# Kernel optimization log

Measured on AMD Instinct MI355X. Metric: run time of the kernel, lower is better.

## Reference

```python
import jax, jax.numpy as jnp
import numpy as np

N_USERS = 50000
N_ENTITIES = 100000
N_EDGES = 2000000
NNZ = 1000000
N_REL = 17  # n_relations; weight has n_relations-1 = 16 rows
DIM = 64
N_HOPS = 3


def setup_inputs() -> dict:
    key = jax.random.key(0)
    ks = jax.random.split(key, 8)
    user_emb = jax.random.normal(ks[0], (N_USERS, DIM), dtype=jnp.float32)
    entity_emb = jax.random.normal(ks[1], (N_ENTITIES, DIM), dtype=jnp.float32)
    weight = jax.random.normal(ks[2], (N_REL - 1, DIM), dtype=jnp.float32)
    unmask = jax.random.uniform(ks[3], (N_EDGES,), dtype=jnp.float32)
    edge_index = jax.random.randint(ks[4], (2, N_EDGES), 0, N_ENTITIES, dtype=jnp.int64) if jax.config.jax_enable_x64 else jax.random.randint(ks[4], (2, N_EDGES), 0, N_ENTITIES).astype(jnp.int32)
    edge_type = jax.random.randint(ks[5], (N_EDGES,), 1, N_REL).astype(edge_index.dtype)
    interact_rows = jax.random.randint(ks[6], (NNZ,), 0, N_USERS).astype(edge_index.dtype)
    interact_cols = jax.random.randint(ks[7], (NNZ,), 0, N_ENTITIES).astype(edge_index.dtype)
    return {
        "user_emb": user_emb,
        "entity_emb": entity_emb,
        "weight": weight,
        "unmask": unmask,
        "edge_index": edge_index,
        "edge_type": edge_type,
        "interact_rows": interact_rows,
        "interact_cols": interact_cols,
    }


def _l2_normalize(x, eps=1e-12):
    # matches torch.nn.functional.normalize(dim=1)
    norm = jnp.sqrt(jnp.sum(x * x, axis=1, keepdims=True))
    return x / jnp.maximum(norm, eps)


def reference(user_emb, entity_emb, weight, unmask, edge_index, edge_type, interact_rows, interact_cols):
    """GraphConv.forward with mess_dropout=False, node_dropout=False (eval math)."""
    head = edge_index[0]
    tail = edge_index[1]
    rel_emb = weight[edge_type - 1]                      # [E, D] gather
    entity_res = entity_emb
    user_res = user_emb
    ent = entity_emb
    for _ in range(N_HOPS):
        # KG aggregate: gather-multiply-scatter_sum
        neigh = ent[tail] * unmask[:, None] * rel_emb    # [E, D]
        ent_agg = jax.ops.segment_sum(neigh, head, num_segments=N_ENTITIES)
        # user aggregate: sparse (unit-valued COO) mm -> gather + segment_sum
        usr_agg = jax.ops.segment_sum(ent[interact_cols], interact_rows, num_segments=N_USERS)
        ent = _l2_normalize(ent_agg)
        usr = _l2_normalize(usr_agg)
        entity_res = entity_res + ent
        user_res = user_res + usr
    return entity_res, user_res
```

## Files before the change

### kernel.cpp

```cpp
#include <hip/hip_runtime.h>
#include <hip/hip_fp16.h>
#include <math.h>

#define N_USERS   50000
#define N_ENT     100000
#define N_EDGES   2000000
#define NNZ       1000000
#define DIM       64
#define N_HOPS    3
#define HALF_E    (N_ENT / 2)
#define HALF_U    (N_USERS / 2)

#define GA     512
#define NB_E   ((N_ENT + 255) >> 8)
#define NB_U   ((N_USERS + 255) >> 8)
#define CAP_D  6400


__device__ inline unsigned pack_h2(float x, float y) {
    unsigned lo = __half_as_ushort(__float2half_rn(x));
    unsigned hi = __half_as_ushort(__float2half_rn(y));
    return lo | (hi << 16);
}

__device__ inline float2 unpack_h2(unsigned u) {
    __half2 h = *reinterpret_cast<__half2*>(&u);
    return __half22float2(h);
}

__global__ void f32_to_f16(const float4* __restrict__ in, uint4* __restrict__ out, int n4) {
    int i = blockIdx.x * blockDim.x + threadIdx.x;
    if (i < n4) {
        float4 a = in[2 * i], b = in[2 * i + 1];
        uint4 o;
        o.x = pack_h2(a.x, a.y);
        o.y = pack_h2(a.z, a.w);
        o.z = pack_h2(b.x, b.y);
        o.w = pack_h2(b.z, b.w);
        out[i] = o;
    }
}


template <int NBUCKET>
__global__ __launch_bounds__(256) void bucket_hist(const int* __restrict__ key, int n,
                                                   int* __restrict__ bh) {
    __shared__ int h[NBUCKET];
    for (int t = threadIdx.x; t < NBUCKET; t += 256) h[t] = 0;
    __syncthreads();
    int chunk = (n + GA - 1) / GA;
    int s = blockIdx.x * chunk;
    int e = n < s + chunk ? n : s + chunk;
    for (int i = s + threadIdx.x; i < e; i += 256)
        atomicAdd(&h[key[i] >> 8], 1);
    __syncthreads();
    for (int t = threadIdx.x; t < NBUCKET; t += 256)
        bh[t * GA + blockIdx.x] = h[t];
}

__global__ void scan_partial(const int* __restrict__ cnt, int n, int* __restrict__ bsum) {
    __shared__ int sd[256];
    int tid = threadIdx.x, i = blockIdx.x * 256 + tid;
    sd[tid] = (i < n) ? cnt[i] : 0;
    __syncthreads();
    for (int s = 128; s > 0; s >>= 1) {
        if (tid < s) sd[tid] += sd[tid + s];
        __syncthreads();
    }
    if (tid == 0) bsum[blockIdx.x] = sd[0];
}

__global__ void scan_bsum(int* bsum, int nb) {
    __shared__ int sd[1024];
    int tid = threadIdx.x;
    int v = (tid < nb) ? bsum[tid] : 0;
    sd[tid] = v;
    __syncthreads();
    for (int o = 1; o < 1024; o <<= 1) {
        int t = (tid >= o) ? sd[tid - o] : 0;
        __syncthreads();
        sd[tid] += t;
        __syncthreads();
    }
    if (tid < nb) bsum[tid] = sd[tid] - v;
}

__global__ void scan_final(const int* __restrict__ cnt, int n,
                           const int* __restrict__ bsum, int* __restrict__ rp) {
    __shared__ int sd[256];
    int tid = threadIdx.x, i = blockIdx.x * 256 + tid;
    int v = (i < n) ? cnt[i] : 0;
    sd[tid] = v;
    __syncthreads();
    for (int o = 1; o < 256; o <<= 1) {
        int t = (tid >= o) ? sd[tid - o] : 0;
        __syncthreads();
        sd[tid] += t;
        __syncthreads();
    }
    int incl = sd[tid] + bsum[blockIdx.x];
    if (i < n) rp[i] = incl - v;
    if (i == n - 1) rp[n] = incl;
}

__global__ __launch_bounds__(256) void bucket_scatter_e(
    const int* __restrict__ head, const int* __restrict__ tail,
    const int* __restrict__ etype, const float* __restrict__ unmask,
    const int* __restrict__ off, long long* __restrict__ tmp) {
    __shared__ int h[NB_E];
    __shared__ int boff[NB_E];
    for (int t = threadIdx.x; t < NB_E; t += 256) { h[t] = 0; boff[t] = off[t * GA + blockIdx.x]; }
    __syncthreads();
    int chunk = (N_EDGES + GA - 1) / GA;
    int s = blockIdx.x * chunk;
    int e = N_EDGES < s + chunk ? N_EDGES : s + chunk;
    for (int i = s + threadIdx.x; i < e; i += 256) {
        int k = head[i];
        int b = k >> 8;
        int local = atomicAdd(&h[b], 1);
        unsigned lo = (unsigned)(tail[i] | ((etype[i] - 1) << 20) | ((k & 255) << 24));
        unsigned hi = (unsigned)__float_as_int(unmask[i]);
        tmp[boff[b] + local] = (long long)(((unsigned long long)hi << 32) | lo);
    }
}

__global__ __launch_bounds__(256) void bucket_scatter_u(
    const int* __restrict__ rows, const int* __restrict__ cols,
    const int* __restrict__ off, int* __restrict__ tmp) {
    __shared__ int h[NB_U];
    __shared__ int boff[NB_U];
    for (int t = threadIdx.x; t < NB_U; t += 256) { h[t] = 0; boff[t] = off[t * GA + blockIdx.x]; }
    __syncthreads();
    int chunk = (NNZ + GA - 1) / GA;
    int s = blockIdx.x * chunk;
    int e = NNZ < s + chunk ? NNZ : s + chunk;
    for (int i = s + threadIdx.x; i < e; i += 256) {
        int k = rows[i];
        int b = k >> 8;
        int local = atomicAdd(&h[b], 1);
        tmp[boff[b] + local] = cols[i] | ((k & 255) << 24);
    }
}

__global__ __launch_bounds__(256) void bucket_sort_e(
    const int* __restrict__ off, const long long* __restrict__ tmp,
    long long* __restrict__ ev, int* __restrict__ rp) {
    __shared__ int khist[256];
    __shared__ int koff[256];
    __shared__ long long stage[CAP_D];
    int b = blockIdx.x;
    int sb = off[b * GA];
    int se = off[(b + 1) * GA];
    int len = se - sb;
    int t = threadIdx.x;
    khist[t] = 0;
    __syncthreads();
    for (int i = t; i < len; i += 256)
        atomicAdd(&khist[(int)(((unsigned long long)tmp[sb + i] >> 24) & 255)], 1);
    __syncthreads();
    int v = khist[t];
    koff[t] = v;
    __syncthreads();
    for (int o = 1; o < 256; o <<= 1) {
        int x = (t >= o) ? koff[t - o] : 0;
        __syncthreads();
        koff[t] += x;
        __syncthreads();
    }
    int excl = koff[t] - v;
    int key = b * 256 + t;
    if (key < N_ENT) rp[key] = sb + excl;
    if (b == 0 && t == 0) rp[N_ENT] = N_EDGES;
    khist[t] = excl;
    __syncthreads();
    if (len <= CAP_D) {
        for (int i = t; i < len; i += 256) {
            long long v2 = tmp[sb + i];
            int k = (int)(((unsigned long long)v2 >> 24) & 255);
            int p = atomicAdd(&khist[k], 1);
            stage[p] = v2;
        }
        __syncthreads();
        for (int i = t; i < len; i += 256)
            ev[sb + i] = stage[i] & (long long)0xFFFFFFFF00FFFFFFULL;
    } else {
        for (int i = t; i < len; i += 256) {
            long long v2 = tmp[sb + i];
            int k = (int)(((unsigned long long)v2 >> 24) & 255);
            int p = atomicAdd(&khist[k], 1);
            ev[sb + p] = v2 & (long long)0xFFFFFFFF00FFFFFFULL;
        }
    }
}

__global__ __launch_bounds__(256) void bucket_sort_u(
    const int* __restrict__ off, const int* __restrict__ tmp,
    int* __restrict__ col_s, int* __restrict__ rp) {
    __shared__ int khist[256];
    __shared__ int koff[256];
    __shared__ int stage[CAP_D];
    int b = blockIdx.x;
    int sb = off[b * GA];
    int se = off[(b + 1) * GA];
    int len = se - sb;
    int t = threadIdx.x;
    khist[t] = 0;
    __syncthreads();
    for (int i = t; i < len; i += 256)
        atomicAdd(&khist[(tmp[sb + i] >> 24) & 255], 1);
    __syncthreads();
    int v = khist[t];
    koff[t] = v;
    __syncthreads();
    for (int o = 1; o < 256; o <<= 1) {
        int x = (t >= o) ? koff[t - o] : 0;
        __syncthreads();
        koff[t] += x;
        __syncthreads();
    }
    int excl = koff[t] - v;
    int key = b * 256 + t;
    if (key < N_USERS) rp[key] = sb + excl;
    if (b == 0 && t == 0) rp[N_USERS] = NNZ;
    khist[t] = excl;
    __syncthreads();
    if (len <= CAP_D) {
        for (int i = t; i < len; i += 256) {
            int v2 = tmp[sb + i];
            int p = atomicAdd(&khist[(v2 >> 24) & 255], 1);
            stage[p] = v2;
        }
        __syncthreads();
        for (int i = t; i < len; i += 256)
            col_s[sb + i] = stage[i] & 0x00FFFFFF;
    } else {
        for (int i = t; i < len; i += 256) {
            int v2 = tmp[sb + i];
            int p = atomicAdd(&khist[(v2 >> 24) & 255], 1);
            col_s[sb + p] = v2 & 0x00FFFFFF;
        }
    }
}


__device__ inline void edge_body(const uint4* __restrict__ in16,
                                 const float4* __restrict__ w32,
                                 int ex, float sc, int sub, float (&acc)[8]) {
    int t = ex & 0xFFFFF, rt = (ex >> 20) & 15;
    uint4 r4 = in16[(size_t)t * 8 + sub];
    float4 wa = w32[rt * 16 + sub * 2];
    float4 wb = w32[rt * 16 + sub * 2 + 1];
    float2 r0 = unpack_h2(r4.x), r1 = unpack_h2(r4.y);
    float2 r2 = unpack_h2(r4.z), r3 = unpack_h2(r4.w);
    acc[0] = fmaf(r0.x * sc, wa.x, acc[0]);
    acc[1] = fmaf(r0.y * sc, wa.y, acc[1]);
    acc[2] = fmaf(r1.x * sc, wa.z, acc[2]);
    acc[3] = fmaf(r1.y * sc, wa.w, acc[3]);
    acc[4] = fmaf(r2.x * sc, wb.x, acc[4]);
    acc[5] = fmaf(r2.y * sc, wb.y, acc[5]);
    acc[6] = fmaf(r3.x * sc, wb.z, acc[6]);
    acc[7] = fmaf(r3.y * sc, wb.w, acc[7]);
}

template <int FINAL>
__global__ __launch_bounds__(256) void agg_hop(
    const uint4* __restrict__ in16, const float4* __restrict__ w32,
    const int* __restrict__ rp_e, const int2* __restrict__ ev,
    const int* __restrict__ rp_u, const int* __restrict__ col_s,
    uint4* __restrict__ oute, uint4* __restrict__ outu,
    const uint4* __restrict__ pe1, const uint4* __restrict__ pu1,
    const uint4* __restrict__ pu2,
    const float4* __restrict__ emb_e, const float4* __restrict__ emb_u,
    float4* __restrict__ res_e, float4* __restrict__ res_u) {
    int gwave = (blockIdx.x * blockDim.x + threadIdx.x) >> 6;
    if (gwave >= HALF_E + HALF_U) return;
    int lane = threadIdx.x & 63;
    int half = lane >> 5;
    int grp = (lane >> 3) & 3;
    int sub = lane & 7;

    bool is_ent = gwave < HALF_E;
    int row = is_ent ? gwave * 2 + half : (gwave - HALF_E) * 2 + half;
    const int* __restrict__ rp = is_ent ? rp_e : rp_u;
    int beg = rp[row], end = rp[row + 1];

    float acc[8];
#pragma unroll
    for (int j = 0; j < 8; ++j) acc[j] = 0.f;

    if (is_ent) {
        for (int p0 = beg; p0 < end; p0 += 8) {
            int pA = p0 + grp, pB = p0 + 4 + grp;
            int2 eA = (pA < end) ? ev[pA] : make_int2(0, 0);
            int2 eB = (pB < end) ? ev[pB] : make_int2(0, 0);
            edge_body(in16, w32, eA.x, __int_as_float(eA.y), sub, acc);
            edge_body(in16, w32, eB.x, __int_as_float(eB.y), sub, acc);
        }
    } else {
        for (int p0 = beg; p0 < end; p0 += 8) {
            int pA = p0 + grp, pB = p0 + 4 + grp;
            int cA = 0, cB = 0;
            float mA = 0.f, mB = 0.f;
            if (pA < end) { cA = col_s[pA]; mA = 1.f; }
            if (pB < end) { cB = col_s[pB]; mB = 1.f; }
            {
                uint4 r4 = in16[(size_t)cA * 8 + sub];
                float2 r0 = unpack_h2(r4.x), r1 = unpack_h2(r4.y);
                float2 r2 = unpack_h2(r4.z), r3 = unpack_h2(r4.w);
                acc[0] = fmaf(r0.x, mA, acc[0]); acc[1] = fmaf(r0.y, mA, acc[1]);
                acc[2] = fmaf(r1.x, mA, acc[2]); acc[3] = fmaf(r1.y, mA, acc[3]);
                acc[4] = fmaf(r2.x, mA, acc[4]); acc[5] = fmaf(r2.y, mA, acc[5]);
                acc[6] = fmaf(r3.x, mA, acc[6]); acc[7] = fmaf(r3.y, mA, acc[7]);
            }
            {
                uint4 r4 = in16[(size_t)cB * 8 + sub];
                float2 r0 = unpack_h2(r4.x), r1 = unpack_h2(r4.y);
                float2 r2 = unpack_h2(r4.z), r3 = unpack_h2(r4.w);
                acc[0] = fmaf(r0.x, mB, acc[0]); acc[1] = fmaf(r0.y, mB, acc[1]);
                acc[2] = fmaf(r1.x, mB, acc[2]); acc[3] = fmaf(r1.y, mB, acc[3]);
                acc[4] = fmaf(r2.x, mB, acc[4]); acc[5] = fmaf(r2.y, mB, acc[5]);
                acc[6] = fmaf(r3.x, mB, acc[6]); acc[7] = fmaf(r3.y, mB, acc[7]);
            }
        }
    }

#pragma unroll
    for (int j = 0; j < 8; ++j) {
        acc[j] += __shfl_xor(acc[j], 8, 64);
        acc[j] += __shfl_xor(acc[j], 16, 64);
    }
    float ss = 0.f;
#pragma unroll
    for (int j = 0; j < 8; ++j) ss = fmaf(acc[j], acc[j], ss);
    ss += __shfl_xor(ss, 1, 64);
    ss += __shfl_xor(ss, 2, 64);
    ss += __shfl_xor(ss, 4, 64);
    float inv = 1.0f / fmaxf(sqrtf(ss), 1e-12f);

    if (grp == 0) {
        float n0 = acc[0] * inv, n1 = acc[1] * inv, n2 = acc[2] * inv, n3 = acc[3] * inv;
        float n4 = acc[4] * inv, n5 = acc[5] * inv, n6 = acc[6] * inv, n7 = acc[7] * inv;
        if constexpr (!FINAL) {
            uint4 p;
            p.x = pack_h2(n0, n1); p.y = pack_h2(n2, n3);
            p.z = pack_h2(n4, n5); p.w = pack_h2(n6, n7);
            (is_ent ? oute : outu)[(size_t)row * 8 + sub] = p;
        } else {
            const uint4* q1p = is_ent ? pe1 : pu1;
            const uint4* q2p = is_ent ? in16 : pu2;
            uint4 q1 = q1p[(size_t)row * 8 + sub];
            uint4 q2 = q2p[(size_t)row * 8 + sub];
            const float4* emb = is_ent ? emb_e : emb_u;
            float4* res = is_ent ? res_e : res_u;
            size_t rb = (size_t)row * 16 + sub * 2;
            float4 a = emb[rb], b = emb[rb + 1];
            float2 x0 = unpack_h2(q1.x), x1 = unpack_h2(q1.y);
            float2 x2 = unpack_h2(q1.z), x3 = unpack_h2(q1.w);
            float2 y0 = unpack_h2(q2.x), y1 = unpack_h2(q2.y);
            float2 y2 = unpack_h2(q2.z), y3 = unpack_h2(q2.w);
            a.x += n0 + x0.x + y0.x;  a.y += n1 + x0.y + y0.y;
            a.z += n2 + x1.x + y1.x;  a.w += n3 + x1.y + y1.y;
            b.x += n4 + x2.x + y2.x;  b.y += n5 + x2.y + y2.y;
            b.z += n6 + x3.x + y3.x;  b.w += n7 + x3.y + y3.y;
            res[rb] = a;
            res[rb + 1] = b;
        }
    }
}


extern "C" void kernel_launch(void* const* d_in, const int* in_sizes, int n_in,
                              void* d_out, int out_size, void* d_ws, size_t ws_size,
                              hipStream_t stream) {
    const float* user_emb   = (const float*)d_in[0];
    const float* entity_emb = (const float*)d_in[1];
    const float* weight     = (const float*)d_in[2];
    const float* unmask     = (const float*)d_in[3];
    const int*   edge_index = (const int*)d_in[4];
    const int*   edge_type  = (const int*)d_in[5];
    const int*   irows      = (const int*)d_in[6];
    const int*   icols      = (const int*)d_in[7];
    const int* head = edge_index;
    const int* tail = edge_index + N_EDGES;

    char* ws = (char*)d_ws;
    size_t off = 0;
    auto alloc = [&](size_t bytes) -> void* {
        void* p = ws + off;
        off += (bytes + 255) & ~(size_t)255;
        return p;
    };
    uint4* B0     = (uint4*)alloc((size_t)N_ENT * DIM * 2);
    uint4* B1     = (uint4*)alloc((size_t)N_ENT * DIM * 2);
    uint4* B2     = (uint4*)alloc((size_t)N_ENT * DIM * 2);
    uint4* U1     = (uint4*)alloc((size_t)N_USERS * DIM * 2);
    uint4* U2     = (uint4*)alloc((size_t)N_USERS * DIM * 2);
    int*   rp_e   = (int*)alloc((N_ENT + 1) * 4);
    int*   rp_u   = (int*)alloc((N_USERS + 1) * 4);
    long long* ev     = (long long*)alloc((size_t)N_EDGES * 8);
    long long* tmp_ev = (long long*)alloc((size_t)N_EDGES * 8);
    int*   col_s   = (int*)alloc((size_t)NNZ * 4);
    int*   tmp_col = (int*)alloc((size_t)NNZ * 4);
    int*   bh_e   = (int*)alloc((size_t)(NB_E * GA + 1) * 4);
    int*   off_e  = (int*)alloc((size_t)(NB_E * GA + 1) * 4);
    int*   bh_u   = (int*)alloc((size_t)(NB_U * GA + 1) * 4);
    int*   off_u  = (int*)alloc((size_t)(NB_U * GA + 1) * 4);
    int*   bs     = (int*)alloc(1024 * 4);
    (void)ws_size;

    f32_to_f16<<<(N_ENT * DIM / 8 + 255) / 256, 256, 0, stream>>>(
        (const float4*)entity_emb, B0, N_ENT * DIM / 8);

    bucket_hist<NB_E><<<GA, 256, 0, stream>>>(head, N_EDGES, bh_e);
    int n_e = NB_E * GA, nb_e = (n_e + 255) / 256;
    scan_partial<<<nb_e, 256, 0, stream>>>(bh_e, n_e, bs);
    scan_bsum<<<1, 1024, 0, stream>>>(bs, nb_e);
    scan_final<<<nb_e, 256, 0, stream>>>(bh_e, n_e, bs, off_e);
    bucket_scatter_e<<<GA, 256, 0, stream>>>(head, tail, edge_type, unmask, off_e, tmp_ev);
    bucket_sort_e<<<NB_E, 256, 0, stream>>>(off_e, tmp_ev, ev, rp_e);

    bucket_hist<NB_U><<<GA, 256, 0, stream>>>(irows, NNZ, bh_u);
    int n_u = NB_U * GA, nb_u = (n_u + 255) / 256;
    scan_partial<<<nb_u, 256, 0, stream>>>(bh_u, n_u, bs);
    scan_bsum<<<1, 1024, 0, stream>>>(bs, nb_u);
    scan_final<<<nb_u, 256, 0, stream>>>(bh_u, n_u, bs, off_u);
    bucket_scatter_u<<<GA, 256, 0, stream>>>(irows, icols, off_u, tmp_col);
    bucket_sort_u<<<NB_U, 256, 0, stream>>>(off_u, tmp_col, col_s, rp_u);

    float* res_e = (float*)d_out;
    float* res_u = res_e + (size_t)N_ENT * DIM;
    const float4* w32 = (const float4*)weight;
    int grid_agg = ((HALF_E + HALF_U) * 64 + 255) / 256;

    agg_hop<0><<<grid_agg, 256, 0, stream>>>(
        B0, w32, rp_e, (const int2*)ev, rp_u, col_s, B1, U1,
        nullptr, nullptr, nullptr, nullptr, nullptr, nullptr, nullptr);
    agg_hop<0><<<grid_agg, 256, 0, stream>>>(
        B1, w32, rp_e, (const int2*)ev, rp_u, col_s, B2, U2,
        nullptr, nullptr, nullptr, nullptr, nullptr, nullptr, nullptr);
    agg_hop<1><<<grid_agg, 256, 0, stream>>>(
        B2, w32, rp_e, (const int2*)ev, rp_u, col_s, nullptr, nullptr,
        B1, U1, U2,
        (const float4*)entity_emb, (const float4*)user_emb,
        (float4*)res_e, (float4*)res_u);
}
```

Measured before the change: 289.6 us.

## Accumulate aggregation in packed half2 and merge entity/user sort kernels

Switches the per-hop gather accumulation from fp32 FMAs on unpacked halves to packed __half2 FMAs. Weights are pre-converted to fp16, and unmask is stored as a duplicated half2 in the edge record. Separately, the entity and user bucket-sort pipelines (histogram, scan, scatter, sort) are merged into single launches over a combined offset array, cutting the number of kernel launches. The half-precision accumulation halves the ALU work per edge but raises the risk of overflow and precision loss when summing many neighbours.

```diff
diff --git a/kernel.cpp b/kernel.cpp
--- a/kernel.cpp
+++ b/kernel.cpp
@@ -7,14 +7,17 @@
 #define N_EDGES   2000000
 #define NNZ       1000000
 #define DIM       64
-#define N_HOPS    3
 #define HALF_E    (N_ENT / 2)
 #define HALF_U    (N_USERS / 2)
 
-#define GA     512
-#define NB_E   ((N_ENT + 255) >> 8)
-#define NB_U   ((N_USERS + 255) >> 8)
-#define CAP_D  6400
+#define GA      512
+#define NB_E    391
+#define NB_U    196
+#define NALL_E  (NB_E * GA)
+#define NALL_U  (NB_U * GA)
+#define NALL    (NALL_E + NALL_U)
+#define NB_SCAN (NALL / 512)
+#define CAP_D   6400
 
 
 __device__ inline unsigned pack_h2(float x, float y) {
@@ -26,6 +29,14 @@
 __device__ inline float2 unpack_h2(unsigned u) {
     __half2 h = *reinterpret_cast<__half2*>(&u);
     return __half22float2(h);
+}
+
+__device__ inline __half2 bits_h2(unsigned u) { return *reinterpret_cast<__half2*>(&u); }
+
+__device__ inline __half2 shfl_h2(__half2 v, int o) {
+    int x = *reinterpret_cast<int*>(&v);
+    x = __shfl_xor(x, o, 64);
+    return *reinterpret_cast<__half2*>(&x);
 }
 
 __global__ void f32_to_f16(const float4* __restrict__ in, uint4* __restrict__ out, int n4) {
@@ -42,28 +53,33 @@
 }
 
 
-template <int NBUCKET>
-__global__ __launch_bounds__(256) void bucket_hist(const int* __restrict__ key, int n,
-                                                   int* __restrict__ bh) {
-    __shared__ int h[NBUCKET];
-    for (int t = threadIdx.x; t < NBUCKET; t += 256) h[t] = 0;
+__global__ __launch_bounds__(256) void bucket_hist_both(
+    const int* __restrict__ head, const int* __restrict__ irows, int* __restrict__ bh) {
+    __shared__ int h[NB_E];
+    bool isE = blockIdx.x < GA;
+    int b = isE ? blockIdx.x : blockIdx.x - GA;
+    const int* key = isE ? head : irows;
+    int n = isE ? N_EDGES : NNZ;
+    int nbuck = isE ? NB_E : NB_U;
+    int base = isE ? 0 : NALL_E;
+    for (int t = threadIdx.x; t < nbuck; t += 256) h[t] = 0;
     __syncthreads();
     int chunk = (n + GA - 1) / GA;
-    int s = blockIdx.x * chunk;
+    int s = b * chunk;
     int e = n < s + chunk ? n : s + chunk;
     for (int i = s + threadIdx.x; i < e; i += 256)
         atomicAdd(&h[key[i] >> 8], 1);
     __syncthreads();
-    for (int t = threadIdx.x; t < NBUCKET; t += 256)
-        bh[t * GA + blockIdx.x] = h[t];
+    for (int t = threadIdx.x; t < nbuck; t += 256)
+        bh[base + t * GA + b] = h[t];
 }
 
 __global__ void scan_partial(const int* __restrict__ cnt, int n, int* __restrict__ bsum) {
-    __shared__ int sd[256];
-    int tid = threadIdx.x, i = blockIdx.x * 256 + tid;
+    __shared__ int sd[512];
+    int tid = threadIdx.x, i = blockIdx.x * 512 + tid;
     sd[tid] = (i < n) ? cnt[i] : 0;
     __syncthreads();
-    for (int s = 128; s > 0; s >>= 1) {
+    for (int s = 256; s > 0; s >>= 1) {
         if (tid < s) sd[tid] += sd[tid + s];
         __syncthreads();
     }
@@ -87,12 +103,12 @@
 
 __global__ void scan_final(const int* __restrict__ cnt, int n,
                            const int* __restrict__ bsum, int* __restrict__ rp) {
-    __shared__ int sd[256];
-    int tid = threadIdx.x, i = blockIdx.x * 256 + tid;
+    __shared__ int sd[512];
+    int tid = threadIdx.x, i = blockIdx.x * 512 + tid;
     int v = (i < n) ? cnt[i] : 0;
     sd[tid] = v;
     __syncthreads();
-    for (int o = 1; o < 256; o <<= 1) {
+    for (int o = 1; o < 512; o <<= 1) {
         int t = (tid >= o) ? sd[tid - o] : 0;
         __syncthreads();
         sd[tid] += t;
@@ -103,168 +119,159 @@
     if (i == n - 1) rp[n] = incl;
 }
 
-__global__ __launch_bounds__(256) void bucket_scatter_e(
+__global__ __launch_bounds__(256) void bucket_scatter_both(
     const int* __restrict__ head, const int* __restrict__ tail,
     const int* __restrict__ etype, const float* __restrict__ unmask,
-    const int* __restrict__ off, long long* __restrict__ tmp) {
+    const int* __restrict__ irows, const int* __restrict__ icols,
+    const int* __restrict__ off, long long* __restrict__ tmp_ev,
+    int* __restrict__ tmp_col) {
     __shared__ int h[NB_E];
     __shared__ int boff[NB_E];
-    for (int t = threadIdx.x; t < NB_E; t += 256) { h[t] = 0; boff[t] = off[t * GA + blockIdx.x]; }
-    __syncthreads();
-    int chunk = (N_EDGES + GA - 1) / GA;
-    int s = blockIdx.x * chunk;
-    int e = N_EDGES < s + chunk ? N_EDGES : s + chunk;
-    for (int i = s + threadIdx.x; i < e; i += 256) {
-        int k = head[i];
-        int b = k >> 8;
-        int local = atomicAdd(&h[b], 1);
-        unsigned lo = (unsigned)(tail[i] | ((etype[i] - 1) << 20) | ((k & 255) << 24));
-        unsigned hi = (unsigned)__float_as_int(unmask[i]);
-        tmp[boff[b] + local] = (long long)(((unsigned long long)hi << 32) | lo);
-    }
-}
-
-__global__ __launch_bounds__(256) void bucket_scatter_u(
-    const int* __restrict__ rows, const int* __restrict__ cols,
-    const int* __restrict__ off, int* __restrict__ tmp) {
-    __shared__ int h[NB_U];
-    __shared__ int boff[NB_U];
-    for (int t = threadIdx.x; t < NB_U; t += 256) { h[t] = 0; boff[t] = off[t * GA + blockIdx.x]; }
-    __syncthreads();
-    int chunk = (NNZ + GA - 1) / GA;
-    int s = blockIdx.x * chunk;
-    int e = NNZ < s + chunk ? NNZ : s + chunk;
-    for (int i = s + threadIdx.x; i < e; i += 256) {
-        int k = rows[i];
-        int b = k >> 8;
-        int local = atomicAdd(&h[b], 1);
-        tmp[boff[b] + local] = cols[i] | ((k & 255) << 24);
-    }
-}
-
-__global__ __launch_bounds__(256) void bucket_sort_e(
-    const int* __restrict__ off, const long long* __restrict__ tmp,
-    long long* __restrict__ ev, int* __restrict__ rp) {
+    bool isE = blockIdx.x < GA;
+    int b = isE ? blockIdx.x : blockIdx.x - GA;
+    if (isE) {
+        for (int t = threadIdx.x; t < NB_E; t += 256) { h[t] = 0; boff[t] = off[t * GA + b]; }
+        __syncthreads();
+        int chunk = (N_EDGES + GA - 1) / GA;
+        int s = b * chunk;
+        int e = N_EDGES < s + chunk ? N_EDGES : s + chunk;
+        for (int i = s + threadIdx.x; i < e; i += 256) {
+            int k = head[i];
+            int bk = k >> 8;
+            int local = atomicAdd(&h[bk], 1);
+            unsigned hh = __half_as_ushort(__float2half_rn(unmask[i]));
+            unsigned hi = hh | (hh << 16);
+            unsigned lo = (unsigned)(tail[i] | ((etype[i] - 1) << 20) | ((k & 255) << 24));
+            tmp_ev[boff[bk] + local] = (long long)(((unsigned long long)hi << 32) | lo);
+        }
+    } else {
+        for (int t = threadIdx.x; t < NB_U; t += 256) { h[t] = 0; boff[t] = off[NALL_E + t * GA + b] - N_EDGES; }
+        __syncthreads();
+        int chunk = (NNZ + GA - 1) / GA;
+        int s = b * chunk;
+        int e = NNZ < s + chunk ? NNZ : s + chunk;
+        for (int i = s + threadIdx.x; i < e; i += 256) {
+            int k = irows[i];
+            int bk = k >> 8;
+            int local = atomicAdd(&h[bk], 1);
+            tmp_col[boff[bk] + local] = icols[i] | ((k & 255) << 24);
+        }
+    }
+}
+
+__global__ __launch_bounds__(256) void bucket_sort_both(
+    const int* __restrict__ off, const long long* __restrict__ tmp_ev,
+    const int* __restrict__ tmp_col, long long* __restrict__ ev,
+    int* __restrict__ col_s, int* __restrict__ rp_e, int* __restrict__ rp_u) {
     __shared__ int khist[256];
     __shared__ int koff[256];
     __shared__ long long stage[CAP_D];
-    int b = blockIdx.x;
-    int sb = off[b * GA];
-    int se = off[(b + 1) * GA];
-    int len = se - sb;
     int t = threadIdx.x;
-    khist[t] = 0;
-    __syncthreads();
-    for (int i = t; i < len; i += 256)
-        atomicAdd(&khist[(int)(((unsigned long long)tmp[sb + i] >> 24) & 255)], 1);
-    __syncthreads();
-    int v = khist[t];
-    koff[t] = v;
-    __syncthreads();
-    for (int o = 1; o < 256; o <<= 1) {
-        int x = (t >= o) ? koff[t - o] : 0;
-        __syncthreads();
-        koff[t] += x;
-        __syncthreads();
-    }
-    int excl = koff[t] - v;
-    int key = b * 256 + t;
-    if (key < N_ENT) rp[key] = sb + excl;
-    if (b == 0 && t == 0) rp[N_ENT] = N_EDGES;
-    khist[t] = excl;
-    __syncthreads();
-    if (len <= CAP_D) {
-        for (int i = t; i < len; i += 256) {
-            long long v2 = tmp[sb + i];
-            int k = (int)(((unsigned long long)v2 >> 24) & 255);
-            int p = atomicAdd(&khist[k], 1);
-            stage[p] = v2;
-        }
+    bool isE = blockIdx.x < NB_E;
+    if (isE) {
+        int b = blockIdx.x;
+        int sb = off[b * GA], se = off[(b + 1) * GA];
+        int len = se - sb;
+        khist[t] = 0;
         __syncthreads();
         for (int i = t; i < len; i += 256)
-            ev[sb + i] = stage[i] & (long long)0xFFFFFFFF00FFFFFFULL;
+            atomicAdd(&khist[(int)(((unsigned long long)tmp_ev[sb + i] >> 24) & 255)], 1);
+        __syncthreads();
+        int v = khist[t];
+        koff[t] = v;
+        __syncthreads();
+        for (int o = 1; o < 256; o <<= 1) {
+            int x = (t >= o) ? koff[t - o] : 0;
+            __syncthreads();
+            koff[t] += x;
+            __syncthreads();
+        }
+        int excl = koff[t] - v;
+        int key = b * 256 + t;
+        if (key < N_ENT) rp_e[key] = sb + excl;
+        if (b == 0 && t == 0) rp_e[N_ENT] = N_EDGES;
+        khist[t] = excl;
+        __syncthreads();
+        if (len <= CAP_D) {
+            for (int i = t; i < len; i += 256) {
+                long long v2 = tmp_ev[sb + i];
+                int k = (int)(((unsigned long long)v2 >> 24) & 255);
+                int p = atomicAdd(&khist[k], 1);
+                stage[p] = v2;
+            }
+            __syncthreads();
+            for (int i = t; i < len; i += 256)
+                ev[sb + i] = stage[i] & (long long)0xFFFFFFFF00FFFFFFULL;
+        } else {
+            for (int i = t; i < len; i += 256) {
+                long long v2 = tmp_ev[sb + i];
+                int k = (int)(((unsigned long long)v2 >> 24) & 255);
+                int p = atomicAdd(&khist[k], 1);
+                ev[sb + p] = v2 & (long long)0xFFFFFFFF00FFFFFFULL;
+            }
+        }
     } else {
-        for (int i = t; i < len; i += 256) {
-            long long v2 = tmp[sb + i];
-            int k = (int)(((unsigned long long)v2 >> 24) & 255);
-            int p = atomicAdd(&khist[k], 1);
-            ev[sb + p] = v2 & (long long)0xFFFFFFFF00FFFFFFULL;
-        }
-    }
-}
-
-__global__ __launch_bounds__(256) void bucket_sort_u(
-    const int* __restrict__ off, const int* __restrict__ tmp,
-    int* __restrict__ col_s, int* __restrict__ rp) {
-    __shared__ int khist[256];
-    __shared__ int koff[256];
-    __shared__ int stage[CAP_D];
-    int b = blockIdx.x;
-    int sb = off[b * GA];
-    int se = off[(b + 1) * GA];
-    int len = se - sb;
-    int t = threadIdx.x;
-    khist[t] = 0;
-    __syncthreads();
-    for (int i = t; i < len; i += 256)
-        atomicAdd(&khist[(tmp[sb + i] >> 24) & 255], 1);
-    __syncthreads();
-    int v = khist[t];
-    koff[t] = v;
-    __syncthreads();
-    for (int o = 1; o < 256; o <<= 1) {
-        int x = (t >= o) ? koff[t - o] : 0;
-        __syncthreads();
-        koff[t] += x;
-        __syncthreads();
-    }
-    int excl = koff[t] - v;
-    int key = b * 256 + t;
-    if (key < N_USERS) rp[key] = sb + excl;
-    if (b == 0 && t == 0) rp[N_USERS] = NNZ;
-    khist[t] = excl;
-    __syncthreads();
-    if (len <= CAP_D) {
-        for (int i = t; i < len; i += 256) {
-            int v2 = tmp[sb + i];
-            int p = atomicAdd(&khist[(v2 >> 24) & 255], 1);
-            stage[p] = v2;
-        }
+        int b = blockIdx.x - NB_E;
+        int sb = off[NALL_E + b * GA] - N_EDGES;
+        int se = off[NALL_E + (b + 1) * GA] - N_EDGES;
+        int len = se - sb;
+        int* stage32 = (int*)stage;
+        khist[t] = 0;
         __syncthreads();
         for (int i = t; i < len; i += 256)
-            col_s[sb + i] = stage[i] & 0x00FFFFFF;
-    } else {
-        for (int i = t; i < len; i += 256) {
-            int v2 = tmp[sb + i];
-            int p = atomicAdd(&khist[(v2 >> 24) & 255], 1);
-            col_s[sb + p] = v2 & 0x00FFFFFF;
-        }
-    }
-}
-
-
-__device__ inline void edge_body(const uint4* __restrict__ in16,
-                                 const float4* __restrict__ w32,
-                                 int ex, float sc, int sub, float (&acc)[8]) {
-    int t = ex & 0xFFFFF, rt = (ex >> 20) & 15;
-    uint4 r4 = in16[(size_t)t * 8 + sub];
-    float4 wa = w32[rt * 16 + sub * 2];
-    float4 wb = w32[rt * 16 + sub * 2 + 1];
-    float2 r0 = unpack_h2(r4.x), r1 = unpack_h2(r4.y);
-    float2 r2 = unpack_h2(r4.z), r3 = unpack_h2(r4.w);
-    acc[0] = fmaf(r0.x * sc, wa.x, acc[0]);
-    acc[1] = fmaf(r0.y * sc, wa.y, acc[1]);
-    acc[2] = fmaf(r1.x * sc, wa.z, acc[2]);
-    acc[3] = fmaf(r1.y * sc, wa.w, acc[3]);
-    acc[4] = fmaf(r2.x * sc, wb.x, acc[4]);
-    acc[5] = fmaf(r2.y * sc, wb.y, acc[5]);
-    acc[6] = fmaf(r3.x * sc, wb.z, acc[6]);
-    acc[7] = fmaf(r3.y * sc, wb.w, acc[7]);
+            atomicAdd(&khist[(tmp_col[sb + i] >> 24) & 255], 1);
+        __syncthreads();
+        int v = khist[t];
+        koff[t] = v;
+        __syncthreads();
+        for (int o = 1; o < 256; o <<= 1) {
+            int x = (t >= o) ? koff[t - o] : 0;
+            __syncthreads();
+            koff[t] += x;
+            __syncthreads();
+        }
+        int excl = koff[t] - v;
+        int key = b * 256 + t;
+        if (key < N_USERS) rp_u[key] = sb + excl;
+        if (b == 0 && t == 0) rp_u[N_USERS] = NNZ;
+        khist[t] = excl;
+        __syncthreads();
+        if (len <= CAP_D) {
+            for (int i = t; i < len; i += 256) {
+                int v2 = tmp_col[sb + i];
+                int p = atomicAdd(&khist[(v2 >> 24) & 255], 1);
+                stage32[p] = v2;
+            }
+            __syncthreads();
+            for (int i = t; i < len; i += 256)
+                col_s[sb + i] = stage32[i] & 0x00FFFFFF;
+        } else {
+            for (int i = t; i < len; i += 256) {
+                int v2 = tmp_col[sb + i];
+                int p = atomicAdd(&khist[(v2 >> 24) & 255], 1);
+                col_s[sb + p] = v2 & 0x00FFFFFF;
+            }
+        }
+    }
+}
+
+
+__device__ inline void edge_body16(const uint4* __restrict__ in16,
+                                   const uint4* __restrict__ w16,
+                                   int ex, unsigned scbits, int sub, __half2 (&acc)[4]) {
+    int tt = ex & 0xFFFFF, rt = (ex >> 20) & 15;
+    uint4 r4 = in16[(size_t)tt * 8 + sub];
+    uint4 w4 = w16[rt * 8 + sub];
+    __half2 sc2 = bits_h2(scbits);
+    acc[0] = __hfma2(__hmul2(bits_h2(r4.x), sc2), bits_h2(w4.x), acc[0]);
+    acc[1] = __hfma2(__hmul2(bits_h2(r4.y), sc2), bits_h2(w4.y), acc[1]);
+    acc[2] = __hfma2(__hmul2(bits_h2(r4.z), sc2), bits_h2(w4.z), acc[2]);
+    acc[3] = __hfma2(__hmul2(bits_h2(r4.w), sc2), bits_h2(w4.w), acc[3]);
 }
 
 template <int FINAL>
 __global__ __launch_bounds__(256) void agg_hop(
-    const uint4* __restrict__ in16, const float4* __restrict__ w32,
+    const uint4* __restrict__ in16, const uint4* __restrict__ w16,
     const int* __restrict__ rp_e, const int2* __restrict__ ev,
     const int* __restrict__ rp_u, const int* __restrict__ col_s,
     uint4* __restrict__ oute, uint4* __restrict__ outu,
@@ -284,62 +291,60 @@
     const int* __restrict__ rp = is_ent ? rp_e : rp_u;
     int beg = rp[row], end = rp[row + 1];
 
-    float acc[8];
+    __half2 acc[4];
 #pragma unroll
-    for (int j = 0; j < 8; ++j) acc[j] = 0.f;
+    for (int j = 0; j < 4; ++j) acc[j] = bits_h2(0u);
 
     if (is_ent) {
         for (int p0 = beg; p0 < end; p0 += 8) {
             int pA = p0 + grp, pB = p0 + 4 + grp;
             int2 eA = (pA < end) ? ev[pA] : make_int2(0, 0);
             int2 eB = (pB < end) ? ev[pB] : make_int2(0, 0);
-            edge_body(in16, w32, eA.x, __int_as_float(eA.y), sub, acc);
-            edge_body(in16, w32, eB.x, __int_as_float(eB.y), sub, acc);
+            edge_body16(in16, w16, eA.x, (unsigned)eA.y, sub, acc);
+            edge_body16(in16, w16, eB.x, (unsigned)eB.y, sub, acc);
         }
     } else {
         for (int p0 = beg; p0 < end; p0 += 8) {
             int pA = p0 + grp, pB = p0 + 4 + grp;
             int cA = 0, cB = 0;
-            float mA = 0.f, mB = 0.f;
-            if (pA < end) { cA = col_s[pA]; mA = 1.f; }
-            if (pB < end) { cB = col_s[pB]; mB = 1.f; }
+            unsigned mAb = 0u, mBb = 0u;
+            if (pA < end) { cA = col_s[pA]; mAb = 0x3C003C00u; }
+            if (pB < end) { cB = col_s[pB]; mBb = 0x3C003C00u; }
+            __half2 mA = bits_h2(mAb), mB = bits_h2(mBb);
             {
                 uint4 r4 = in16[(size_t)cA * 8 + sub];
-                float2 r0 = unpack_h2(r4.x), r1 = unpack_h2(r4.y);
-                float2 r2 = unpack_h2(r4.z), r3 = unpack_h2(r4.w);
-                acc[0] = fmaf(r0.x, mA, acc[0]); acc[1] = fmaf(r0.y, mA, acc[1]);
-                acc[2] = fmaf(r1.x, mA, acc[2]); acc[3] = fmaf(r1.y, mA, acc[3]);
-                acc[4] = fmaf(r2.x, mA, acc[4]); acc[5] = fmaf(r2.y, mA, acc[5]);
-                acc[6] = fmaf(r3.x, mA, acc[6]); acc[7] = fmaf(r3.y, mA, acc[7]);
+                acc[0] = __hfma2(bits_h2(r4.x), mA, acc[0]);
+                acc[1] = __hfma2(bits_h2(r4.y), mA, acc[1]);
+                acc[2] = __hfma2(bits_h2(r4.z), mA, acc[2]);
+                acc[3] = __hfma2(bits_h2(r4.w), mA, acc[3]);
             }
             {
                 uint4 r4 = in16[(size_t)cB * 8 + sub];
-                float2 r0 = unpack_h2(r4.x), r1 = unpack_h2(r4.y);
-                float2 r2 = unpack_h2(r4.z), r3 = unpack_h2(r4.w);
-                acc[0] = fmaf(r0.x, mB, acc[0]); acc[1] = fmaf(r0.y, mB, acc[1]);
-                acc[2] = fmaf(r1.x, mB, acc[2]); acc[3] = fmaf(r1.y, mB, acc[3]);
-                acc[4] = fmaf(r2.x, mB, acc[4]); acc[5] = fmaf(r2.y, mB, acc[5]);
-                acc[6] = fmaf(r3.x, mB, acc[6]); acc[7] = fmaf(r3.y, mB, acc[7]);
+                acc[0] = __hfma2(bits_h2(r4.x), mB, acc[0]);
+                acc[1] = __hfma2(bits_h2(r4.y), mB, acc[1]);
+                acc[2] = __hfma2(bits_h2(r4.z), mB, acc[2]);
+                acc[3] = __hfma2(bits_h2(r4.w), mB, acc[3]);
             }
         }
     }
 
 #pragma unroll
-    for (int j = 0; j < 8; ++j) {
-        acc[j] += __shfl_xor(acc[j], 8, 64);
-        acc[j] += __shfl_xor(acc[j], 16, 64);
-    }
-    float ss = 0.f;
-#pragma unroll
-    for (int j = 0; j < 8; ++j) ss = fmaf(acc[j], acc[j], ss);
+    for (int j = 0; j < 4; ++j) {
+        acc[j] = __hadd2(acc[j], shfl_h2(acc[j], 8));
+        acc[j] = __hadd2(acc[j], shfl_h2(acc[j], 16));
+    }
+    float2 f0 = __half22float2(acc[0]), f1 = __half22float2(acc[1]);
+    float2 f2 = __half22float2(acc[2]), f3 = __half22float2(acc[3]);
+    float ss = f0.x * f0.x + f0.y * f0.y + f1.x * f1.x + f1.y * f1.y +
+               f2.x * f2.x + f2.y * f2.y + f3.x * f3.x + f3.y * f3.y;
     ss += __shfl_xor(ss, 1, 64);
     ss += __shfl_xor(ss, 2, 64);
     ss += __shfl_xor(ss, 4, 64);
     float inv = 1.0f / fmaxf(sqrtf(ss), 1e-12f);
 
     if (grp == 0) {
-        float n0 = acc[0] * inv, n1 = acc[1] * inv, n2 = acc[2] * inv, n3 = acc[3] * inv;
-        float n4 = acc[4] * inv, n5 = acc[5] * inv, n6 = acc[6] * inv, n7 = acc[7] * inv;
+        float n0 = f0.x * inv, n1 = f0.y * inv, n2 = f1.x * inv, n3 = f1.y * inv;
+        float n4 = f2.x * inv, n5 = f2.y * inv, n6 = f3.x * inv, n7 = f3.y * inv;
         if constexpr (!FINAL) {
             uint4 p;
             p.x = pack_h2(n0, n1); p.y = pack_h2(n2, n3);
@@ -395,51 +400,43 @@
     uint4* B2     = (uint4*)alloc((size_t)N_ENT * DIM * 2);
     uint4* U1     = (uint4*)alloc((size_t)N_USERS * DIM * 2);
     uint4* U2     = (uint4*)alloc((size_t)N_USERS * DIM * 2);
+    uint4* w16    = (uint4*)alloc(16 * DIM * 2);
     int*   rp_e   = (int*)alloc((N_ENT + 1) * 4);
     int*   rp_u   = (int*)alloc((N_USERS + 1) * 4);
     long long* ev     = (long long*)alloc((size_t)N_EDGES * 8);
     long long* tmp_ev = (long long*)alloc((size_t)N_EDGES * 8);
     int*   col_s   = (int*)alloc((size_t)NNZ * 4);
     int*   tmp_col = (int*)alloc((size_t)NNZ * 4);
-    int*   bh_e   = (int*)alloc((size_t)(NB_E * GA + 1) * 4);
-    int*   off_e  = (int*)alloc((size_t)(NB_E * GA + 1) * 4);
-    int*   bh_u   = (int*)alloc((size_t)(NB_U * GA + 1) * 4);
-    int*   off_u  = (int*)alloc((size_t)(NB_U * GA + 1) * 4);
+    int*   bh     = (int*)alloc((size_t)(NALL + 1) * 4);
+    int*   offA   = (int*)alloc((size_t)(NALL + 1) * 4);
     int*   bs     = (int*)alloc(1024 * 4);
     (void)ws_size;
 
     f32_to_f16<<<(N_ENT * DIM / 8 + 255) / 256, 256, 0, stream>>>(
         (const float4*)entity_emb, B0, N_ENT * DIM / 8);
-
-    bucket_hist<NB_E><<<GA, 256, 0, stream>>>(head, N_EDGES, bh_e);
-    int n_e = NB_E * GA, nb_e = (n_e + 255) / 256;
-    scan_partial<<<nb_e, 256, 0, stream>>>(bh_e, n_e, bs);
-    scan_bsum<<<1, 1024, 0, stream>>>(bs, nb_e);
-    scan_final<<<nb_e, 256, 0, stream>>>(bh_e, n_e, bs, off_e);
-    bucket_scatter_e<<<GA, 256, 0, stream>>>(head, tail, edge_type, unmask, off_e, tmp_ev);
-    bucket_sort_e<<<NB_E, 256, 0, stream>>>(off_e, tmp_ev, ev, rp_e);
-
-    bucket_hist<NB_U><<<GA, 256, 0, stream>>>(irows, NNZ, bh_u);
-    int n_u = NB_U * GA, nb_u = (n_u + 255) / 256;
-    scan_partial<<<nb_u, 256, 0, stream>>>(bh_u, n_u, bs);
-    scan_bsum<<<1, 1024, 0, stream>>>(bs, nb_u);
-    scan_final<<<nb_u, 256, 0, stream>>>(bh_u, n_u, bs, off_u);
-    bucket_scatter_u<<<GA, 256, 0, stream>>>(irows, icols, off_u, tmp_col);
-    bucket_sort_u<<<NB_U, 256, 0, stream>>>(off_u, tmp_col, col_s, rp_u);
+    f32_to_f16<<<1, 128, 0, stream>>>((const float4*)weight, w16, 16 * DIM / 8);
+
+    bucket_hist_both<<<2 * GA, 256, 0, stream>>>(head, irows, bh);
+    scan_partial<<<NB_SCAN, 512, 0, stream>>>(bh, NALL, bs);
+    scan_bsum<<<1, 1024, 0, stream>>>(bs, NB_SCAN);
+    scan_final<<<NB_SCAN, 512, 0, stream>>>(bh, NALL, bs, offA);
+    bucket_scatter_both<<<2 * GA, 256, 0, stream>>>(
+        head, tail, edge_type, unmask, irows, icols, offA, tmp_ev, tmp_col);
+    bucket_sort_both<<<NB_E + NB_U, 256, 0, stream>>>(
+        offA, tmp_ev, tmp_col, ev, col_s, rp_e, rp_u);
 
     float* res_e = (float*)d_out;
     float* res_u = res_e + (size_t)N_ENT * DIM;
-    const float4* w32 = (const float4*)weight;
     int grid_agg = ((HALF_E + HALF_U) * 64 + 255) / 256;
 
     agg_hop<0><<<grid_agg, 256, 0, stream>>>(
-        B0, w32, rp_e, (const int2*)ev, rp_u, col_s, B1, U1,
+        B0, w16, rp_e, (const int2*)ev, rp_u, col_s, B1, U1,
         nullptr, nullptr, nullptr, nullptr, nullptr, nullptr, nullptr);
     agg_hop<0><<<grid_agg, 256, 0, stream>>>(
-        B1, w32, rp_e, (const int2*)ev, rp_u, col_s, B2, U2,
+        B1, w16, rp_e, (const int2*)ev, rp_u, col_s, B2, U2,
         nullptr, nullptr, nullptr, nullptr, nullptr, nullptr, nullptr);
     agg_hop<1><<<grid_agg, 256, 0, stream>>>(
-        B2, w32, rp_e, (const int2*)ev, rp_u, col_s, nullptr, nullptr,
+        B2, w16, rp_e, (const int2*)ev, rp_u, col_s, nullptr, nullptr,
         B1, U1, U2,
         (const float4*)entity_emb, (const float4*)user_emb,
         (float4*)res_e, (float4*)res_u);
```

Result: faster. 248.1 us (median of 2 runs) (-14.3%).
